# Kernel tuning notes

Measured on AMD Instinct MI355X. Metric: run time of the kernel, lower is better.

## Reference

```python
import jax, jax.numpy as jnp
import numpy as np

N = 100000        # nodes
E = 1_600_000     # edges (avg degree 16)
F_IN = 128        # in_channels
HID = 64          # hidden_channels (per-head)
H1 = 4            # heads layer 1
G = 128           # number of graphs
NEG_SLOPE = 0.2   # PyG GATConv default leaky_relu slope


def setup_inputs() -> dict:
    key = jax.random.key(0)
    ks = jax.random.split(key, 12)
    x = jax.random.normal(ks[0], (N, F_IN), dtype=jnp.float32)
    edge_index = jax.random.randint(ks[1], (2, E), 0, N, dtype=jnp.int64)
    batch = jnp.sort(jax.random.randint(ks[2], (N,), 0, G, dtype=jnp.int64))
    s1 = 1.0 / np.sqrt(F_IN)
    s2 = 1.0 / np.sqrt(H1 * HID)
    # layer 1: in=F_IN, out=H1*HID (PyG lin has no bias; separate bias after concat)
    w1 = jax.random.normal(ks[3], (H1 * HID, F_IN), dtype=jnp.float32) * s1
    a_src1 = jax.random.normal(ks[4], (H1, HID), dtype=jnp.float32) * s1
    a_dst1 = jax.random.normal(ks[5], (H1, HID), dtype=jnp.float32) * s1
    b1 = jnp.zeros((H1 * HID,), dtype=jnp.float32)
    # layer 2: in=H1*HID, out=HID, heads=1
    w2 = jax.random.normal(ks[6], (1 * HID, H1 * HID), dtype=jnp.float32) * s2
    a_src2 = jax.random.normal(ks[7], (1, HID), dtype=jnp.float32) * s2
    a_dst2 = jax.random.normal(ks[8], (1, HID), dtype=jnp.float32) * s2
    b2 = jnp.zeros((HID,), dtype=jnp.float32)
    return {"x": x, "w1": w1, "a_src1": a_src1, "a_dst1": a_dst1, "b1": b1,
            "w2": w2, "a_src2": a_src2, "a_dst2": a_dst2, "b2": b2,
            "edge_index": edge_index, "batch": batch}


def _segment_softmax(alpha, seg, n):
    # numerically-stable softmax of alpha [E,H] grouped by seg (dst node)
    m = jax.ops.segment_max(alpha, seg, num_segments=n)
    m = jnp.where(jnp.isfinite(m), m, 0.0)  # empty segments -> 0
    a = jnp.exp(alpha - m[seg])
    s = jax.ops.segment_sum(a, seg, num_segments=n)
    return a / (s[seg] + 1e-16)


def _gat_conv(x, w, a_src, a_dst, bias, src, dst, n, heads, ch):
    h = (x @ w.T).reshape(n, heads, ch)          # [N,H,C]
    alpha_src = jnp.sum(h * a_src[None], axis=-1)  # [N,H]
    alpha_dst = jnp.sum(h * a_dst[None], axis=-1)  # [N,H]
    e = jax.nn.leaky_relu(alpha_src[src] + alpha_dst[dst], NEG_SLOPE)  # [E,H]
    att = _segment_softmax(e, dst, n)             # [E,H]
    msg = h[src] * att[:, :, None]                # [E,H,C]
    out = jax.ops.segment_sum(msg, dst, num_segments=n)  # [N,H,C]
    return out.reshape(n, heads * ch) + bias


def reference(x, w1, a_src1, a_dst1, b1, w2, a_src2, a_dst2, b2, edge_index, batch):
    src, dst = edge_index[0], edge_index[1]
    h = jax.nn.relu(_gat_conv(x, w1, a_src1, a_dst1, b1, src, dst, N, H1, HID))
    h = jax.nn.relu(_gat_conv(h, w2, a_src2, a_dst2, b2, src, dst, N, 1, HID))
    # global_mean_pool over graph ids
    sums = jax.ops.segment_sum(h, batch, num_segments=G)            # [G,HID]
    cnt = jax.ops.segment_sum(jnp.ones((N,), h.dtype), batch, num_segments=G)
    return sums / jnp.maximum(cnt, 1.0)[:, None]
```

## Files before the change

### kernel.cpp

```cpp
#include <hip/hip_runtime.h>
#include <math.h>
#include <type_traits>

#define NNODES 100000
#define NEDGES 1600000
#define NGRAPH 128
#define NBKT 391
#define CAP 1536
#define EPB 2048

typedef _Float16 f16x4 __attribute__((ext_vector_type(4)));
typedef _Float16 f16x8 __attribute__((ext_vector_type(8)));
typedef float f32x4 __attribute__((ext_vector_type(4)));

__global__ __launch_bounds__(256) void front1(
    const float* __restrict__ w1, const float* __restrict__ w2,
    const float* __restrict__ as1c, const float* __restrict__ ad1c,
    const float* __restrict__ as2c, const float* __restrict__ ad2c,
    _Float16* __restrict__ w1h, _Float16* __restrict__ w2h,
    _Float16* __restrict__ va1, _Float16* __restrict__ va2,
    const int* __restrict__ srcv, const int* __restrict__ dstv,
    unsigned* __restrict__ part, int* __restrict__ gcur, int e_count) {
  __shared__ int hist[NBKT];
  __shared__ int base_[NBKT];
  __shared__ int lofs[NBKT];
  const int tid = threadIdx.x;
  if (blockIdx.x < 202) {
    const int b = blockIdx.x;
    if (b < 8) {
      if (tid < 128) {
        int h = b & 3;
        const float* coef = (b >= 4) ? ad1c : as1c;
        float s = 0.f;
        for (int c = 0; c < 64; ++c)
          s = fmaf(w1[(size_t)(h * 64 + c) * 128 + tid], coef[h * 64 + c], s);
        va1[b * 128 + tid] = (_Float16)s;
        va1[(b + 8) * 128 + tid] = (_Float16)0.f;
      }
    } else if (b < 10) {
      int r = b - 8;
      const float* coef = r ? ad2c : as2c;
      float s = 0.f;
      for (int c = 0; c < 64; ++c) s = fmaf(w2[(size_t)c * 256 + tid], coef[c], s);
      va2[r * 256 + tid] = (_Float16)s;
      for (int z = 2 + r * 7; z < 9 + r * 7; ++z) va2[z * 256 + tid] = (_Float16)0.f;
    } else if (b < 138) {
      int i = (b - 10) * 256 + tid;
      w1h[i] = (_Float16)w1[i];
    } else {
      int i = (b - 138) * 256 + tid;
      w2h[i] = (_Float16)w2[i];
    }
    return;
  }
  const int ab = blockIdx.x - 202;
  const int P = ab & 7;
  for (int i = tid; i < NBKT; i += 256) { hist[i] = 0; lofs[i] = 0; }
  __syncthreads();
  const int e0 = ab * EPB;
  const int e1 = min(e0 + EPB, e_count);
  for (int e = e0 + tid; e < e1; e += 256) atomicAdd(&hist[dstv[e] >> 8], 1);
  __syncthreads();
  for (int i = tid; i < NBKT; i += 256) {
    int c = hist[i];
    base_[i] = c ? atomicAdd(&gcur[(P * NBKT + i) * 16], c) : 0;
  }
  __syncthreads();
  for (int e = e0 + tid; e < e1; e += 256) {
    int d = dstv[e];
    int b = d >> 8;
    int l = atomicAdd(&lofs[b], 1);
    part[(size_t)(P * NBKT + b) * CAP + base_[b] + l] =
        ((unsigned)srcv[e] << 8) | (unsigned)(d & 255);
  }
}

__global__ __launch_bounds__(256) void bucketB1p(const unsigned* __restrict__ part,
    const int* __restrict__ gcur, int* __restrict__ pre, int* __restrict__ bsum, int n) {
  __shared__ int cnt[256];
  __shared__ int sc[256];
  const int b = blockIdx.x, tid = threadIdx.x;
  cnt[tid] = 0;
  __syncthreads();
  for (int P = 0; P < 8; ++P) {
    int cn = gcur[(P * NBKT + b) * 16];
    const unsigned* seg = part + (size_t)(P * NBKT + b) * CAP;
    for (int i = tid; i < cn; i += 256) atomicAdd(&cnt[seg[i] & 255], 1);
  }
  __syncthreads();
  int own = cnt[tid];
  sc[tid] = own;
  __syncthreads();
  for (int o = 1; o < 256; o <<= 1) {
    int t = (tid >= o) ? sc[tid - o] : 0;
    __syncthreads();
    sc[tid] += t;
    __syncthreads();
  }
  int node = (b << 8) + tid;
  if (node < n) pre[node] = sc[tid] - own;
  if (tid == 255) bsum[b] = sc[255];
}

__global__ __launch_bounds__(256) void bucketB2(const unsigned* __restrict__ part,
    const int* __restrict__ gcur, const int* __restrict__ pre,
    const int* __restrict__ bsum, int* __restrict__ offsets,
    int* __restrict__ esrc, int n, int e_count) {
  __shared__ int bs[NBKT];
  __shared__ int red[256];
  __shared__ int lcur[256];
  const int b = blockIdx.x, tid = threadIdx.x;
  for (int i = tid; i < NBKT; i += 256) bs[i] = bsum[i];
  __syncthreads();
  int part_ = 0;
  for (int i = tid; i < b; i += 256) part_ += bs[i];
  red[tid] = part_;
  __syncthreads();
  for (int o = 128; o; o >>= 1) {
    if (tid < o) red[tid] += red[tid + o];
    __syncthreads();
  }
  int base = red[0];
  int node = (b << 8) + tid;
  int ofs = base;
  if (node < n) {
    ofs = base + pre[node];
    offsets[node] = ofs;
  }
  lcur[tid] = ofs;
  if (b == NBKT - 1 && tid == 0) offsets[n] = e_count;
  __syncthreads();
  for (int P = 0; P < 8; ++P) {
    int cn = gcur[(P * NBKT + b) * 16];
    const unsigned* seg = part + (size_t)(P * NBKT + b) * CAP;
    for (int i = tid; i < cn; i += 256) {
      unsigned e = seg[i];
      int slot = atomicAdd(&lcur[e & 255], 1);
      esrc[slot] = (int)(e >> 8);
    }
  }
}

template <int K, int N, typename AT>
__global__ __launch_bounds__(256) void gemm_mfma(const AT* __restrict__ A,
    const _Float16* __restrict__ Bh, const _Float16* __restrict__ VA,
    _Float16* __restrict__ C, int M, float* __restrict__ asrc, float* __restrict__ adst) {
  constexpr int H = N / 64;
  constexpr int KS = K / 32, NT = N / 16;
  constexpr int BM = 400, NG = 7;
  constexpr int CP = N + 8;
  __shared__ _Float16 Bs[N * K];
  __shared__ _Float16 VAs[16 * K];
  __shared__ _Float16 Cs[64 * CP];
  const int tid = threadIdx.x;
  const int lane = tid & 63, wid = tid >> 6;
  const int lr = lane & 15, lk = (lane >> 4) * 8;
  const int bm = blockIdx.x * BM;

  for (int i = tid * 8; i < N * K; i += 2048) {
    int row = i / K, k = i & (K - 1);
    f16x8 v = *(const f16x8*)&Bh[i];
    *(f16x8*)&Bs[(row * K + k) ^ ((row & 7) << 3)] = v;
  }
  for (int i = tid * 8; i < 16 * K; i += 2048) {
    int row = i / K, k = i & (K - 1);
    f16x8 v = *(const f16x8*)&VA[i];
    *(f16x8*)&VAs[(row * K + k) ^ ((row & 7) << 3)] = v;
  }
  __syncthreads();

  auto loadA = [&](int g, f16x8* areg) {
    int rlocal = g * 64 + wid * 16 + lr;
    int row = bm + rlocal;
    if (rlocal < BM && row < M) {
      const AT* arow = A + (size_t)row * K;
#pragma unroll
      for (int ks = 0; ks < KS; ++ks) {
        if constexpr (std::is_same<AT, float>::value) {
          float4 v0 = *(const float4*)&arow[ks * 32 + lk];
          float4 v1 = *(const float4*)&arow[ks * 32 + lk + 4];
          f16x8 t;
          t[0] = (_Float16)v0.x; t[1] = (_Float16)v0.y; t[2] = (_Float16)v0.z; t[3] = (_Float16)v0.w;
          t[4] = (_Float16)v1.x; t[5] = (_Float16)v1.y; t[6] = (_Float16)v1.z; t[7] = (_Float16)v1.w;
          areg[ks] = t;
        } else {
          areg[ks] = *(const f16x8*)&arow[ks * 32 + lk];
        }
      }
    } else {
#pragma unroll
      for (int ks = 0; ks < KS; ++ks) areg[ks] = (f16x8){};
    }
  };

  f16x8 a[KS], an[KS];
  loadA(0, a);
  const int rl0 = wid * 16 + (lane >> 4) * 4;

  for (int g = 0; g < NG; ++g) {
    if (g + 1 < NG) loadA(g + 1, an);

    f32x4 accv = (f32x4){0.f, 0.f, 0.f, 0.f};
#pragma unroll
    for (int ks = 0; ks < KS; ++ks) {
      f16x8 bv = *(const f16x8*)&VAs[(lr * K + ks * 32 + lk) ^ ((lr & 7) << 3)];
      accv = __builtin_amdgcn_mfma_f32_16x16x32_f16(a[ks], bv, accv, 0, 0, 0);
    }

    f32x4 acc[NT];
#pragma unroll
    for (int nt = 0; nt < NT; ++nt) acc[nt] = (f32x4){0.f, 0.f, 0.f, 0.f};
#pragma unroll
    for (int nt = 0; nt < NT; ++nt) {
      int brow = nt * 16 + lr;
#pragma unroll
      for (int ks = 0; ks < KS; ++ks) {
        f16x8 b = *(const f16x8*)&Bs[(brow * K + ks * 32 + lk) ^ ((brow & 7) << 3)];
        acc[nt] = __builtin_amdgcn_mfma_f32_16x16x32_f16(a[ks], b, acc[nt], 0, 0, 0);
      }
    }

#pragma unroll
    for (int r = 0; r < 4; ++r) {
      int rl = rl0 + r;
#pragma unroll
      for (int nt = 0; nt < NT; ++nt) Cs[rl * CP + nt * 16 + lr] = (_Float16)acc[nt][r];
      int rlocal = g * 64 + rl;
      int row = bm + rlocal;
      if (rlocal < BM && row < M) {
        if (lr < H) asrc[row * H + lr] = accv[r];
        else if (lr < 2 * H) adst[row * H + lr - H] = accv[r];
      }
    }
    __syncthreads();

    int rmax = min(64, min(BM - g * 64, M - (bm + g * 64)));
    if (rmax > 0) {
      int nch = rmax * (N / 8);
      for (int q = tid; q < nch; q += 256) {
        int row = q / (N / 8), c8 = q % (N / 8);
        f16x8 v = *(const f16x8*)&Cs[row * CP + c8 * 8];
        *(f16x8*)&C[(size_t)(bm + g * 64 + row) * N + c8 * 8] = v;
      }
    }
    __syncthreads();
#pragma unroll
    for (int ks = 0; ks < KS; ++ks) a[ks] = an[ks];
  }
}

__global__ __launch_bounds__(256, 8) void agg1_kernel(const _Float16* __restrict__ hmat,
    const float* __restrict__ asrc, const float* __restrict__ adst,
    const int* __restrict__ offsets, const int* __restrict__ esrc,
    const float* __restrict__ bias, _Float16* __restrict__ outv, int node0) {
  const int lane = threadIdx.x & 63, wid = threadIdx.x >> 6;
  const int node = node0 + blockIdx.x * 4 + wid;
  if (node >= NNODES) return;
  const int h = lane >> 4;
  const int start = offsets[node];
  const int end = offsets[node + 1];
  const float adn = adst[node * 4 + h];
  const _Float16* hbase = hmat + lane * 4;
  float acc[4] = {0.f, 0.f, 0.f, 0.f};
  float s = 0.f;
  int j = start;
  for (; j + 8 <= end; j += 8) {
    int sv[8];
#pragma unroll
    for (int t = 0; t < 8; ++t) sv[t] = esrc[j + t];
    f16x4 vv[8];
#pragma unroll
    for (int t = 0; t < 8; ++t) vv[t] = *(const f16x4*)&hbase[(size_t)sv[t] * 256];
    _Float16 ph[8];
#pragma unroll
    for (int t = 0; t < 8; ++t) {
      float v = asrc[sv[t] * 4 + h] + adn;
      v = (v > 0.f) ? v : 0.2f * v;
      float p = __expf(v);
      s += p;
      ph[t] = (_Float16)p;
    }
#pragma unroll
    for (int t = 0; t < 8; ++t)
#pragma unroll
      for (int k = 0; k < 4; ++k)
        acc[k] = fmaf((float)vv[t][k], (float)ph[t], acc[k]);
  }
  for (; j < end; ++j) {
    int sv = esrc[j];
    f16x4 vv = *(const f16x4*)&hbase[(size_t)sv * 256];
    float v = asrc[sv * 4 + h] + adn;
    v = (v > 0.f) ? v : 0.2f * v;
    float p = __expf(v);
    s += p;
    _Float16 phs = (_Float16)p;
#pragma unroll
    for (int k = 0; k < 4; ++k) acc[k] = fmaf((float)vv[k], (float)phs, acc[k]);
  }
  float inv = 1.f / (s + 1e-16f);
  f16x4 ho;
#pragma unroll
  for (int k = 0; k < 4; ++k)
    ho[k] = (_Float16)fmaxf(fmaf(acc[k], inv, bias[lane * 4 + k]), 0.f);
  *(f16x4*)&outv[(size_t)node * 256 + lane * 4] = ho;
}

__global__ __launch_bounds__(256, 8) void agg2_kernel(const _Float16* __restrict__ hmat,
    const float* __restrict__ asrc, const float* __restrict__ adst,
    const int* __restrict__ offsets, const int* __restrict__ esrc,
    const float* __restrict__ bias, _Float16* __restrict__ outv) {
  const int lane = threadIdx.x & 63, wid = threadIdx.x >> 6;
  const int g = lane >> 4, q = lane & 15;
  const int node = blockIdx.x * 16 + wid * 4 + g;
  if (node >= NNODES) return;
  const int start = offsets[node];
  const int end = offsets[node + 1];
  const float adn = adst[node];
  const _Float16* hbase = hmat + q * 4;
  float acc[4] = {0.f, 0.f, 0.f, 0.f};
  float s = 0.f;
  int j = start;
  for (; j + 8 <= end; j += 8) {
    int sv[8];
#pragma unroll
    for (int t = 0; t < 8; ++t) sv[t] = esrc[j + t];
    f16x4 v[8];
#pragma unroll
    for (int t = 0; t < 8; ++t) v[t] = *(const f16x4*)&hbase[(size_t)sv[t] * 64];
#pragma unroll
    for (int t = 0; t < 8; ++t) {
      float x = asrc[sv[t]] + adn;
      x = (x > 0.f) ? x : 0.2f * x;
      float p = __expf(x);
      s += p;
      _Float16 phs = (_Float16)p;
#pragma unroll
      for (int k = 0; k < 4; ++k) acc[k] = fmaf((float)v[t][k], (float)phs, acc[k]);
    }
  }
  for (; j < end; ++j) {
    int sv = esrc[j];
    f16x4 v = *(const f16x4*)&hbase[(size_t)sv * 64];
    float x = asrc[sv] + adn;
    x = (x > 0.f) ? x : 0.2f * x;
    float p = __expf(x);
    s += p;
    _Float16 phs = (_Float16)p;
#pragma unroll
    for (int k = 0; k < 4; ++k) acc[k] = fmaf((float)v[k], (float)phs, acc[k]);
  }
  float inv = 1.f / (s + 1e-16f);
  f16x4 ho;
#pragma unroll
  for (int k = 0; k < 4; ++k)
    ho[k] = (_Float16)fmaxf(fmaf(acc[k], inv, bias[q * 4 + k]), 0.f);
  *(f16x4*)&outv[(size_t)node * 64 + q * 4] = ho;
}

__global__ __launch_bounds__(256) void pool_kernel(const _Float16* __restrict__ g2,
    const int* __restrict__ batch, float* __restrict__ out, int n) {
  const int gid = blockIdx.x;
  const int lane = threadIdx.x & 63, w = threadIdx.x >> 6;
  int lo = 0, hi = n;
  while (lo < hi) { int mid = (lo + hi) >> 1; if (batch[mid] < gid) lo = mid + 1; else hi = mid; }
  int lb = lo;
  hi = n;
  while (lo < hi) { int mid = (lo + hi) >> 1; if (batch[mid] < gid + 1) lo = mid + 1; else hi = mid; }
  int ub = lo;
  float acc = 0.f;
  for (int i = lb + w; i < ub; i += 4) acc += (float)g2[(size_t)i * 64 + lane];
  __shared__ float red[4][64];
  red[w][lane] = acc;
  __syncthreads();
  if (threadIdx.x < 64) {
    float sum = (red[0][lane] + red[1][lane]) + (red[2][lane] + red[3][lane]);
    float cnt = fmaxf((float)(ub - lb), 1.f);
    out[gid * 64 + lane] = sum / cnt;
  }
}

extern "C" void kernel_launch(void* const* d_in, const int* in_sizes, int n_in,
                              void* d_out, int out_size, void* d_ws, size_t ws_size,
                              hipStream_t stream) {
  const float* x      = (const float*)d_in[0];
  const float* w1     = (const float*)d_in[1];
  const float* a_src1 = (const float*)d_in[2];
  const float* a_dst1 = (const float*)d_in[3];
  const float* b1     = (const float*)d_in[4];
  const float* w2     = (const float*)d_in[5];
  const float* a_src2 = (const float*)d_in[6];
  const float* a_dst2 = (const float*)d_in[7];
  const float* b2     = (const float*)d_in[8];
  const int*   src    = (const int*)d_in[9];
  const int*   dst    = src + NEDGES;
  const int*   batch  = (const int*)d_in[10];
  float* out = (float*)d_out;

  const int N = NNODES, E = NEDGES;

  char* wsb = (char*)d_ws;
  size_t off = 0;
  auto alloc = [&](size_t bytes) {
    void* p = wsb + off;
    off = (off + bytes + 255) & ~(size_t)255;
    return p;
  };
  _Float16* h1h = (_Float16*)alloc((size_t)N * 256 * 2);
  _Float16* g1h = (_Float16*)alloc((size_t)N * 256 * 2);
  _Float16* h2h = (_Float16*)alloc((size_t)N * 64 * 2);
  _Float16* g2h = (_Float16*)alloc((size_t)N * 64 * 2);
  float* as1    = (float*)alloc((size_t)N * 4 * 4);
  float* ad1    = (float*)alloc((size_t)N * 4 * 4);
  float* as2    = (float*)alloc((size_t)N * 4);
  float* ad2    = (float*)alloc((size_t)N * 4);
  int* pre      = (int*)alloc((size_t)N * 4);
  int* bsum     = (int*)alloc((size_t)NBKT * 4);
  int* offsets  = (int*)alloc((size_t)(N + 1) * 4);
  int* esrc     = (int*)alloc((size_t)E * 4);
  unsigned* part= (unsigned*)alloc((size_t)8 * NBKT * CAP * 4);
  int* gcur     = (int*)alloc((size_t)8 * NBKT * 16 * 4);
  _Float16* w1h = (_Float16*)alloc((size_t)256 * 128 * 2);
  _Float16* w2h = (_Float16*)alloc((size_t)64 * 256 * 2);
  _Float16* va1 = (_Float16*)alloc((size_t)16 * 128 * 2);
  _Float16* va2 = (_Float16*)alloc((size_t)16 * 256 * 2);

  hipMemsetAsync(gcur, 0, (size_t)8 * NBKT * 16 * 4, stream);
  front1<<<202 + (E + EPB - 1) / EPB, 256, 0, stream>>>(
      w1, w2, a_src1, a_dst1, a_src2, a_dst2, w1h, w2h, va1, va2,
      src, dst, part, gcur, E);

  bucketB1p<<<NBKT, 256, 0, stream>>>(part, gcur, pre, bsum, N);
  bucketB2<<<NBKT, 256, 0, stream>>>(part, gcur, pre, bsum, offsets, esrc, N, E);

  gemm_mfma<128, 256, float><<<250, 256, 0, stream>>>(
      x, w1h, va1, h1h, N, as1, ad1);
  agg1_kernel<<<12500, 256, 0, stream>>>(h1h, as1, ad1, offsets, esrc, b1, g1h, 0);
  agg1_kernel<<<12500, 256, 0, stream>>>(h1h, as1, ad1, offsets, esrc, b1, g1h, 50000);

  gemm_mfma<256, 64, _Float16><<<250, 256, 0, stream>>>(
      g1h, w2h, va2, h2h, N, as2, ad2);
  agg2_kernel<<<(N + 15) / 16, 256, 0, stream>>>(h2h, as2, ad2, offsets, esrc, b2, g2h);

  pool_kernel<<<NGRAPH, 256, 0, stream>>>(g2h, batch, out, N);
}
```

Baseline: 352.4 us.

## Shrink GEMM epilogue staging buffer, merge agg1 launches, relax launch bounds

The GEMM epilogue now stages output through a 16-row shared buffer, one wave's tile at a time, instead of a 64-row buffer. This cuts shared memory per block, which should let more blocks fit per CU, but it adds four barrier pairs per row group. The two half-range agg1 launches are merged into a single launch, removing one launch and the node offset argument. The occupancy hint of 8 is dropped from the launch bounds of both aggregation kernels, giving the compiler more register freedom at the possible cost of occupancy.

```diff
diff --git a/kernel.cpp b/kernel.cpp
--- a/kernel.cpp
+++ b/kernel.cpp
@@ -151,7 +151,7 @@
   constexpr int CP = N + 8;
   __shared__ _Float16 Bs[N * K];
   __shared__ _Float16 VAs[16 * K];
-  __shared__ _Float16 Cs[64 * CP];
+  __shared__ _Float16 Cs[16 * CP];
   const int tid = threadIdx.x;
   const int lane = tid & 63, wid = tid >> 6;
   const int lr = lane & 15, lk = (lane >> 4) * 8;
@@ -195,7 +195,6 @@
 
   f16x8 a[KS], an[KS];
   loadA(0, a);
-  const int rl0 = wid * 16 + (lane >> 4) * 4;
 
   for (int g = 0; g < NG; ++g) {
     if (g + 1 < NG) loadA(g + 1, an);
@@ -222,39 +221,49 @@
 
 #pragma unroll
     for (int r = 0; r < 4; ++r) {
-      int rl = rl0 + r;
-#pragma unroll
-      for (int nt = 0; nt < NT; ++nt) Cs[rl * CP + nt * 16 + lr] = (_Float16)acc[nt][r];
-      int rlocal = g * 64 + rl;
+      int rlocal = g * 64 + wid * 16 + (lane >> 4) * 4 + r;
       int row = bm + rlocal;
       if (rlocal < BM && row < M) {
         if (lr < H) asrc[row * H + lr] = accv[r];
         else if (lr < 2 * H) adst[row * H + lr - H] = accv[r];
       }
     }
-    __syncthreads();
-
-    int rmax = min(64, min(BM - g * 64, M - (bm + g * 64)));
-    if (rmax > 0) {
-      int nch = rmax * (N / 8);
-      for (int q = tid; q < nch; q += 256) {
-        int row = q / (N / 8), c8 = q % (N / 8);
-        f16x8 v = *(const f16x8*)&Cs[row * CP + c8 * 8];
-        *(f16x8*)&C[(size_t)(bm + g * 64 + row) * N + c8 * 8] = v;
-      }
-    }
-    __syncthreads();
+
+    for (int q = 0; q < 4; ++q) {
+      int qrows = min(16, BM - g * 64 - q * 16);
+      if (qrows <= 0) break;
+      if (wid == q) {
+#pragma unroll
+        for (int r = 0; r < 4; ++r) {
+          int rl = (lane >> 4) * 4 + r;
+#pragma unroll
+          for (int nt = 0; nt < NT; ++nt) Cs[rl * CP + nt * 16 + lr] = (_Float16)acc[nt][r];
+        }
+      }
+      __syncthreads();
+      int rbase = bm + g * 64 + q * 16;
+      int rmax = min(qrows, M - rbase);
+      if (rmax > 0) {
+        int nch = rmax * (N / 8);
+        for (int idx = tid; idx < nch; idx += 256) {
+          int row = idx / (N / 8), c8 = idx % (N / 8);
+          f16x8 v = *(const f16x8*)&Cs[row * CP + c8 * 8];
+          *(f16x8*)&C[(size_t)(rbase + row) * N + c8 * 8] = v;
+        }
+      }
+      __syncthreads();
+    }
 #pragma unroll
     for (int ks = 0; ks < KS; ++ks) a[ks] = an[ks];
   }
 }
 
-__global__ __launch_bounds__(256, 8) void agg1_kernel(const _Float16* __restrict__ hmat,
+__global__ __launch_bounds__(256) void agg1_kernel(const _Float16* __restrict__ hmat,
     const float* __restrict__ asrc, const float* __restrict__ adst,
     const int* __restrict__ offsets, const int* __restrict__ esrc,
-    const float* __restrict__ bias, _Float16* __restrict__ outv, int node0) {
+    const float* __restrict__ bias, _Float16* __restrict__ outv) {
   const int lane = threadIdx.x & 63, wid = threadIdx.x >> 6;
-  const int node = node0 + blockIdx.x * 4 + wid;
+  const int node = blockIdx.x * 4 + wid;
   if (node >= NNODES) return;
   const int h = lane >> 4;
   const int start = offsets[node];
@@ -305,7 +314,7 @@
   *(f16x4*)&outv[(size_t)node * 256 + lane * 4] = ho;
 }
 
-__global__ __launch_bounds__(256, 8) void agg2_kernel(const _Float16* __restrict__ hmat,
+__global__ __launch_bounds__(256) void agg2_kernel(const _Float16* __restrict__ hmat,
     const float* __restrict__ asrc, const float* __restrict__ adst,
     const int* __restrict__ offsets, const int* __restrict__ esrc,
     const float* __restrict__ bias, _Float16* __restrict__ outv) {
@@ -434,8 +443,7 @@
 
   gemm_mfma<128, 256, float><<<250, 256, 0, stream>>>(
       x, w1h, va1, h1h, N, as1, ad1);
-  agg1_kernel<<<12500, 256, 0, stream>>>(h1h, as1, ad1, offsets, esrc, b1, g1h, 0);
-  agg1_kernel<<<12500, 256, 0, stream>>>(h1h, as1, ad1, offsets, esrc, b1, g1h, 50000);
+  agg1_kernel<<<(N + 3) / 4, 256, 0, stream>>>(h1h, as1, ad1, offsets, esrc, b1, g1h);
 
   gemm_mfma<256, 64, _Float16><<<250, 256, 0, stream>>>(
       g1h, w2h, va2, h2h, N, as2, ad2);
```

After: 351.9 us. No clear change (-0.2%).
